# Kernel optimization log

Hardware: AMD Instinct MI355X
Metric: run time of the kernel (lower is better)

Reference implementation:

```python
import jax, jax.numpy as jnp
import numpy as np

QMAX = 127.0  # int8 symmetric
EPS = 1e-8

def _quant_dequant(v, axis):
    # symmetric int8 fake-quant along `axis` (per-row for weights, per-token for acts)
    scale = jnp.max(jnp.abs(v), axis=axis, keepdims=True) / QMAX
    scale = jnp.maximum(scale, EPS)
    q = jnp.clip(jnp.round(v / scale), -QMAX, QMAX)
    return q * scale

def _ste(v, axis):
    # straight-through estimator: identity gradient through quantization
    return v + jax.lax.stop_gradient(_quant_dequant(v, axis) - v)

def setup_inputs() -> dict:
    key = jax.random.key(0)
    k1, k2, k3 = jax.random.split(key, 3)
    H, I = 2048, 5632
    x = jax.random.normal(k1, (4, 2048, H), dtype=jnp.float32)
    # nn.Linear weight layout: [out_features, in_features]
    w_gate_up = jax.random.normal(k2, (2 * I, H), dtype=jnp.float32) * (H ** -0.5)
    w_down = jax.random.normal(k3, (H, I), dtype=jnp.float32) * (I ** -0.5)
    return {"x": x, "w_gate_up": w_gate_up, "w_down": w_down}

def reference(x, w_gate_up, w_down):
    I = w_down.shape[1]
    # QLinear #1: quantize act per-token, weight per-out-channel, dequant matmul
    xq = _ste(x, axis=-1)                       # [B,S,H]
    w1q = _ste(w_gate_up, axis=-1)              # [2I,H]
    gate_up = jnp.einsum('bsh,oh->bso', xq, w1q)  # [B,S,2I]
    gate, up = gate_up[..., :I], gate_up[..., I:]
    h = jax.nn.silu(gate) * up                  # SwiGLU, [B,S,I]
    # QLinear #2
    hq = _ste(h, axis=-1)
    w2q = _ste(w_down, axis=-1)                 # [H,I]
    return jnp.einsum('bsi,oi->bso', hq, w2q)   # [B,S,H]
```

## Files before the change

kernel.cpp:

```cpp
#include <hip/hip_runtime.h>
#include <hip/hip_bf16.h>
#include <stdint.h>

#define H_DIM 2048
#define I_DIM 5632
#define M_DIM 8192
#define N1_DIM (2 * I_DIM)

typedef __attribute__((ext_vector_type(4))) int i32x4;

__device__ __forceinline__ void gload16(const void* g, void* l) {
  __builtin_amdgcn_global_load_lds(
      reinterpret_cast<const __attribute__((address_space(1))) uint32_t*>(
          reinterpret_cast<uintptr_t>(g)),
      reinterpret_cast<__attribute__((address_space(3))) uint32_t*>(
          reinterpret_cast<uintptr_t>(l)),
      16, 0, 0);
}

__global__ __launch_bounds__(256) void quant_rows_f32(
    const float* __restrict__ in, int8_t* __restrict__ q,
    float* __restrict__ scl, int rowlen) {
  const int row = blockIdx.x;
  const int tid = threadIdx.x;
  const float* rp = in + (size_t)row * rowlen;
  float m = 0.f;
  for (int i = tid * 4; i < rowlen; i += 1024) {
    const float4 v = *reinterpret_cast<const float4*>(rp + i);
    m = fmaxf(m, fmaxf(fmaxf(fabsf(v.x), fabsf(v.y)),
                       fmaxf(fabsf(v.z), fabsf(v.w))));
  }
#pragma unroll
  for (int o = 32; o; o >>= 1) m = fmaxf(m, __shfl_xor(m, o));
  __shared__ float wm[4];
  if ((tid & 63) == 0) wm[tid >> 6] = m;
  __syncthreads();
  m = fmaxf(fmaxf(wm[0], wm[1]), fmaxf(wm[2], wm[3]));
  const float scale = fmaxf(m / 127.0f, 1e-8f);
  const float inv = 1.0f / scale;
  if (tid == 0) scl[row] = scale;
  int8_t* qp = q + (size_t)row * rowlen;
  for (int i = tid * 4; i < rowlen; i += 1024) {
    const float4 v = *reinterpret_cast<const float4*>(rp + i);
    const int a = (int)rintf(fminf(fmaxf(v.x * inv, -127.f), 127.f));
    const int b = (int)rintf(fminf(fmaxf(v.y * inv, -127.f), 127.f));
    const int c = (int)rintf(fminf(fmaxf(v.z * inv, -127.f), 127.f));
    const int d = (int)rintf(fminf(fmaxf(v.w * inv, -127.f), 127.f));
    *reinterpret_cast<int*>(qp + i) =
        (a & 255) | ((b & 255) << 8) | ((c & 255) << 16) | (d << 24);
  }
}

__global__ __launch_bounds__(256) void quant_h_rows(
    const __hip_bfloat16* __restrict__ h, const int* __restrict__ amax,
    int8_t* __restrict__ q, float* __restrict__ scl) {
  const int row = blockIdx.x;
  const int tid = threadIdx.x;
  const float scale = fmaxf(__int_as_float(amax[row]) / 127.0f, 1e-8f);
  const float inv = 1.0f / scale;
  if (tid == 0) scl[row] = scale;
  const __hip_bfloat16* rp = h + (size_t)row * I_DIM;
  int8_t* qp = q + (size_t)row * I_DIM;
  for (int i = tid * 8; i < I_DIM; i += 2048) {
    const uint4 v = *reinterpret_cast<const uint4*>(rp + i);
    const uint32_t w[4] = {v.x, v.y, v.z, v.w};
    int pk0 = 0, pk1 = 0;
#pragma unroll
    for (int j = 0; j < 8; ++j) {
      const float f =
          __uint_as_float(((w[j >> 1] >> ((j & 1) * 16)) & 0xffffu) << 16);
      const int qv = (int)rintf(fminf(fmaxf(f * inv, -127.f), 127.f));
      if (j < 4) pk0 |= (qv & 255) << ((j & 3) * 8);
      else       pk1 |= (qv & 255) << ((j & 3) * 8);
    }
    *reinterpret_cast<int2*>(qp + i) = make_int2(pk0, pk1);
  }
}

__global__ __launch_bounds__(256) void gemm1_silu(
    const int8_t* __restrict__ qx, const float* __restrict__ sx,
    const int8_t* __restrict__ qw, const float* __restrict__ sw,
    __hip_bfloat16* __restrict__ h, int* __restrict__ hmax) {
  __shared__ int8_t lds[65536];
  const int tid = threadIdx.x;
  const int lane = tid & 63;
  const int wid = tid >> 6;
  const int bn = blockIdx.x;
  const int bm = blockIdx.y;

  const int lr = lane >> 3;
  const int swz = ((lane & 7) ^ lr) << 4;
  const size_t loff = (size_t)lr * H_DIM + swz;

  const int8_t* Ag  = qx + (size_t)(bm * 128 + wid * 32) * H_DIM;
  const int8_t* Bgg = qw + (size_t)(bn * 64 + wid * 16) * H_DIM;
  const int8_t* Bug = qw + (size_t)(I_DIM + bn * 64 + wid * 16) * H_DIM;

  const int wr = wid >> 1, wc = wid & 1;
  const int c16 = lane & 15;
  const int kq = lane >> 4;
  const int r7 = lane & 7;

  i32x4 accg[4][2] = {};
  i32x4 accu[4][2] = {};

  auto stage = [&](int buf, int kt) {
    const int kb = kt * 128;
#pragma unroll
    for (int i = 0; i < 4; ++i)
      gload16(Ag + (size_t)i * 8 * H_DIM + kb + loff,
              lds + buf * 16384 + (wid * 32 + i * 8) * 128);
#pragma unroll
    for (int i = 0; i < 2; ++i)
      gload16(Bgg + (size_t)i * 8 * H_DIM + kb + loff,
              lds + 32768 + buf * 8192 + (wid * 16 + i * 8) * 128);
#pragma unroll
    for (int i = 0; i < 2; ++i)
      gload16(Bug + (size_t)i * 8 * H_DIM + kb + loff,
              lds + 49152 + buf * 8192 + (wid * 16 + i * 8) * 128);
  };

  stage(0, 0);
  __syncthreads();
  const int KT = H_DIM / 128;
  for (int kt = 0; kt < KT; ++kt) {
    const int cur = kt & 1;
    if (kt + 1 < KT) stage(cur ^ 1, kt + 1);
    const int8_t* Ab  = lds + cur * 16384;
    const int8_t* Bgb = lds + 32768 + cur * 8192;
    const int8_t* Bub = lds + 49152 + cur * 8192;
#pragma unroll
    for (int kk = 0; kk < 2; ++kk) {
      const int slot = ((kk * 4 + kq) ^ r7) << 4;
      i32x4 a[4], bg[2], bu[2];
#pragma unroll
      for (int m = 0; m < 4; ++m)
        a[m] = *reinterpret_cast<const i32x4*>(
            Ab + (wr * 64 + m * 16 + c16) * 128 + slot);
#pragma unroll
      for (int n = 0; n < 2; ++n) {
        bg[n] = *reinterpret_cast<const i32x4*>(
            Bgb + (wc * 32 + n * 16 + c16) * 128 + slot);
        bu[n] = *reinterpret_cast<const i32x4*>(
            Bub + (wc * 32 + n * 16 + c16) * 128 + slot);
      }
#pragma unroll
      for (int m = 0; m < 4; ++m)
#pragma unroll
        for (int n = 0; n < 2; ++n) {
          accg[m][n] =
              __builtin_amdgcn_mfma_i32_16x16x64_i8(a[m], bg[n], accg[m][n], 0, 0, 0);
          accu[m][n] =
              __builtin_amdgcn_mfma_i32_16x16x64_i8(a[m], bu[n], accu[m][n], 0, 0, 0);
        }
    }
    __syncthreads();
  }

  const int row0 = bm * 128 + wr * 64;
  const int col0 = bn * 64 + wc * 32;
#pragma unroll
  for (int m = 0; m < 4; ++m) {
#pragma unroll
    for (int r = 0; r < 4; ++r) {
      const int row = row0 + m * 16 + kq * 4 + r;
      const float sxr = sx[row];
      float rmax = 0.f;
#pragma unroll
      for (int n = 0; n < 2; ++n) {
        const int col = col0 + n * 16 + c16;
        const float g = (float)accg[m][n][r] * (sxr * sw[col]);
        const float u = (float)accu[m][n][r] * (sxr * sw[I_DIM + col]);
        const float hv = g / (1.f + __expf(-g)) * u;
        h[(size_t)row * I_DIM + col] = __float2bfloat16(hv);
        rmax = fmaxf(rmax, fabsf(hv));
      }
#pragma unroll
      for (int o = 1; o < 16; o <<= 1) rmax = fmaxf(rmax, __shfl_xor(rmax, o));
      if (c16 == 0) atomicMax(hmax + row, __float_as_int(rmax));
    }
  }
}

__global__ __launch_bounds__(256) void gemm2(
    const int8_t* __restrict__ qh, const float* __restrict__ sh,
    const int8_t* __restrict__ qw, const float* __restrict__ sw,
    float* __restrict__ out) {
  __shared__ int8_t lds[65536];
  const int tid = threadIdx.x;
  const int lane = tid & 63;
  const int wid = tid >> 6;
  const int bn = blockIdx.x;
  const int bm = blockIdx.y;

  const int lr = lane >> 3;
  const int swz = ((lane & 7) ^ lr) << 4;
  const size_t loff = (size_t)lr * I_DIM + swz;

  const int8_t* Ag = qh + (size_t)(bm * 128 + wid * 32) * I_DIM;
  const int8_t* Bg = qw + (size_t)(bn * 128 + wid * 32) * I_DIM;

  const int wr = wid >> 1, wc = wid & 1;
  const int c16 = lane & 15;
  const int kq = lane >> 4;
  const int r7 = lane & 7;

  i32x4 acc[4][4] = {};

  auto stage = [&](int buf, int kt) {
    const int kb = kt * 128;
#pragma unroll
    for (int i = 0; i < 4; ++i)
      gload16(Ag + (size_t)i * 8 * I_DIM + kb + loff,
              lds + buf * 16384 + (wid * 32 + i * 8) * 128);
#pragma unroll
    for (int i = 0; i < 4; ++i)
      gload16(Bg + (size_t)i * 8 * I_DIM + kb + loff,
              lds + 32768 + buf * 16384 + (wid * 32 + i * 8) * 128);
  };

  stage(0, 0);
  __syncthreads();
  const int KT = I_DIM / 128;
  for (int kt = 0; kt < KT; ++kt) {
    const int cur = kt & 1;
    if (kt + 1 < KT) stage(cur ^ 1, kt + 1);
    const int8_t* Ab = lds + cur * 16384;
    const int8_t* Bb = lds + 32768 + cur * 16384;
#pragma unroll
    for (int kk = 0; kk < 2; ++kk) {
      const int slot = ((kk * 4 + kq) ^ r7) << 4;
      i32x4 a[4], b[4];
#pragma unroll
      for (int m = 0; m < 4; ++m)
        a[m] = *reinterpret_cast<const i32x4*>(
            Ab + (wr * 64 + m * 16 + c16) * 128 + slot);
#pragma unroll
      for (int n = 0; n < 4; ++n)
        b[n] = *reinterpret_cast<const i32x4*>(
            Bb + (wc * 64 + n * 16 + c16) * 128 + slot);
#pragma unroll
      for (int m = 0; m < 4; ++m)
#pragma unroll
        for (int n = 0; n < 4; ++n)
          acc[m][n] =
              __builtin_amdgcn_mfma_i32_16x16x64_i8(a[m], b[n], acc[m][n], 0, 0, 0);
    }
    __syncthreads();
  }

  const int row0 = bm * 128 + wr * 64;
  const int col0 = bn * 128 + wc * 64;
#pragma unroll
  for (int m = 0; m < 4; ++m) {
#pragma unroll
    for (int r = 0; r < 4; ++r) {
      const int row = row0 + m * 16 + kq * 4 + r;
      const float shr = sh[row];
#pragma unroll
      for (int n = 0; n < 4; ++n) {
        const int col = col0 + n * 16 + c16;
        out[(size_t)row * H_DIM + col] = (float)acc[m][n][r] * (shr * sw[col]);
      }
    }
  }
}

extern "C" void kernel_launch(void* const* d_in, const int* in_sizes, int n_in,
                              void* d_out, int out_size, void* d_ws, size_t ws_size,
                              hipStream_t stream) {
  (void)in_sizes; (void)n_in; (void)out_size; (void)ws_size;
  const float* x  = (const float*)d_in[0];
  const float* w1 = (const float*)d_in[1];
  const float* w2 = (const float*)d_in[2];
  float* out = (float*)d_out;

  size_t off = 0;
  auto alloc = [&](size_t n) {
    void* p = (char*)d_ws + off;
    off += (n + 255) & ~(size_t)255;
    return p;
  };
  int8_t* qx  = (int8_t*)alloc((size_t)M_DIM * H_DIM);
  int8_t* qw1 = (int8_t*)alloc((size_t)N1_DIM * H_DIM);
  int8_t* qw2 = (int8_t*)alloc((size_t)H_DIM * I_DIM);
  int8_t* qh  = (int8_t*)alloc((size_t)M_DIM * I_DIM);
  __hip_bfloat16* hb = (__hip_bfloat16*)alloc((size_t)M_DIM * I_DIM * 2);
  float* sx  = (float*)alloc((size_t)M_DIM * 4);
  float* sw1 = (float*)alloc((size_t)N1_DIM * 4);
  float* sw2 = (float*)alloc((size_t)H_DIM * 4);
  float* shs = (float*)alloc((size_t)M_DIM * 4);
  int* hmax  = (int*)alloc((size_t)M_DIM * 4);

  hipMemsetAsync(hmax, 0, (size_t)M_DIM * 4, stream);
  quant_rows_f32<<<M_DIM, 256, 0, stream>>>(x, qx, sx, H_DIM);
  quant_rows_f32<<<N1_DIM, 256, 0, stream>>>(w1, qw1, sw1, H_DIM);
  quant_rows_f32<<<H_DIM, 256, 0, stream>>>(w2, qw2, sw2, I_DIM);
  gemm1_silu<<<dim3(I_DIM / 64, M_DIM / 128), 256, 0, stream>>>(
      qx, sx, qw1, sw1, hb, hmax);
  quant_h_rows<<<M_DIM, 256, 0, stream>>>(hb, hmax, qh, shs);
  gemm2<<<dim3(H_DIM / 128, M_DIM / 128), 256, 0, stream>>>(
      qh, shs, qw2, sw2, out);
}
```

Baseline: 467.7 us.

## Enlarge GEMM tiles to 256x256 with 8 waves and a quarter-split barrier pipeline

Both int8 GEMMs move from 128-row tiles with 4 waves to 256x256 output tiles (gate and up halves together in gemm1) computed by 512-thread blocks. Each K step is split into four MFMA quadrants, with global-to-LDS staging of the next halves interleaved between barriers and priority raised around MFMA bursts. A 1D grid with an XCD-aware block swizzle replaces the 2D grid, aiming to raise operand reuse and L2 locality. The trade-offs are 128KB of LDS per block, a large accumulator register footprint, and many extra barriers.

```diff
diff --git a/kernel.cpp b/kernel.cpp
--- a/kernel.cpp
+++ b/kernel.cpp
@@ -17,6 +17,13 @@
           reinterpret_cast<uintptr_t>(l)),
       16, 0, 0);
 }
+
+#define BAR()                                \
+  do {                                       \
+    asm volatile("" ::: "memory");           \
+    __builtin_amdgcn_s_barrier();            \
+    asm volatile("" ::: "memory");           \
+  } while (0)
 
 __global__ __launch_bounds__(256) void quant_rows_f32(
     const float* __restrict__ in, int8_t* __restrict__ q,
@@ -77,190 +84,283 @@
   }
 }
 
-__global__ __launch_bounds__(256) void gemm1_silu(
+__global__ __launch_bounds__(512, 2) void gemm1_silu(
     const int8_t* __restrict__ qx, const float* __restrict__ sx,
     const int8_t* __restrict__ qw, const float* __restrict__ sw,
     __hip_bfloat16* __restrict__ h, int* __restrict__ hmax) {
-  __shared__ int8_t lds[65536];
+  __shared__ int8_t lds[131072];
   const int tid = threadIdx.x;
   const int lane = tid & 63;
   const int wid = tid >> 6;
-  const int bn = blockIdx.x;
-  const int bm = blockIdx.y;
-
-  const int lr = lane >> 3;
-  const int swz = ((lane & 7) ^ lr) << 4;
-  const size_t loff = (size_t)lr * H_DIM + swz;
-
-  const int8_t* Ag  = qx + (size_t)(bm * 128 + wid * 32) * H_DIM;
-  const int8_t* Bgg = qw + (size_t)(bn * 64 + wid * 16) * H_DIM;
-  const int8_t* Bug = qw + (size_t)(I_DIM + bn * 64 + wid * 16) * H_DIM;
-
-  const int wr = wid >> 1, wc = wid & 1;
+  const int wr = wid >> 2;
+  const int wc = wid & 3;
   const int c16 = lane & 15;
   const int kq = lane >> 4;
   const int r7 = lane & 7;
-
-  i32x4 accg[4][2] = {};
-  i32x4 accu[4][2] = {};
-
-  auto stage = [&](int buf, int kt) {
-    const int kb = kt * 128;
-#pragma unroll
-    for (int i = 0; i < 4; ++i)
-      gload16(Ag + (size_t)i * 8 * H_DIM + kb + loff,
-              lds + buf * 16384 + (wid * 32 + i * 8) * 128);
-#pragma unroll
-    for (int i = 0; i < 2; ++i)
-      gload16(Bgg + (size_t)i * 8 * H_DIM + kb + loff,
-              lds + 32768 + buf * 8192 + (wid * 16 + i * 8) * 128);
-#pragma unroll
-    for (int i = 0; i < 2; ++i)
-      gload16(Bug + (size_t)i * 8 * H_DIM + kb + loff,
-              lds + 49152 + buf * 8192 + (wid * 16 + i * 8) * 128);
-  };
-
-  stage(0, 0);
-  __syncthreads();
+  const int lr = lane >> 3;
+  const int sslot = ((lane & 7) ^ lr) << 4;
+  const int sl0 = (kq ^ r7) << 4;
+  const int sl1 = ((4 + kq) ^ r7) << 4;
+
+  const int nwg = gridDim.x;
+  const int id = blockIdx.x;
+  const int swz = (id & 7) * (nwg >> 3) + (id >> 3);
+  const int NBN = I_DIM / 128;
+  const int bm = swz / NBN;
+  const int bn = swz % NBN;
+
+  const size_t goffA = (size_t)(bm * 256 + wid * 8 + lr) * H_DIM + sslot;
+  const size_t goffG = (size_t)(bn * 128 + wid * 8 + lr) * H_DIM + sslot;
+  const size_t goffU = goffG + (size_t)I_DIM * H_DIM;
+  const int ldsAw = wid * 8 * 128;
+  const int ldsBw = 65536 + wid * 8 * 128;
+
+  i32x4 acc[2][4][2][2] = {};
+
+#define STAGE_A1(half, t)                                                      \
+  do {                                                                         \
+    const int _b = ((t) & 1) * 32768;                                          \
+    _Pragma("unroll") for (int ld = 0; ld < 2; ++ld)                           \
+        gload16(qx + goffA + (size_t)((half)*128 + ld * 64) * H_DIM +          \
+                    (size_t)(t) * 128,                                         \
+                lds + _b + ldsAw + ((half)*128 + ld * 64) * 128);              \
+  } while (0)
+
+#define STAGE_B1(half, t)                                                      \
+  do {                                                                         \
+    const int _b = ((t) & 1) * 32768;                                          \
+    const int8_t* _s = (half) ? (qw + goffU) : (qw + goffG);                   \
+    _Pragma("unroll") for (int ld = 0; ld < 2; ++ld)                           \
+        gload16(_s + (size_t)(ld * 64) * H_DIM + (size_t)(t) * 128,            \
+                lds + _b + ldsBw + ((half)*128 + ld * 64) * 128);              \
+  } while (0)
+
+#define LOAD_A1(MH)                                                            \
+  do {                                                                         \
+    _Pragma("unroll") for (int m = 0; m < 4; ++m) {                            \
+      const int ar = (MH)*128 + wr * 64 + m * 16 + c16;                        \
+      a[m][0] = *reinterpret_cast<const i32x4*>(lds + cb + ar * 128 + sl0);    \
+      a[m][1] = *reinterpret_cast<const i32x4*>(lds + cb + ar * 128 + sl1);    \
+    }                                                                          \
+  } while (0)
+
+#define LOAD_B1(NH)                                                            \
+  do {                                                                         \
+    _Pragma("unroll") for (int n = 0; n < 2; ++n) {                            \
+      const int br = (NH)*128 + wc * 32 + n * 16 + c16;                        \
+      b[NH][n][0] =                                                            \
+          *reinterpret_cast<const i32x4*>(lds + 65536 + cb + br * 128 + sl0);  \
+      b[NH][n][1] =                                                            \
+          *reinterpret_cast<const i32x4*>(lds + 65536 + cb + br * 128 + sl1);  \
+    }                                                                          \
+  } while (0)
+
+#define MFMA_Q1(MH, NH)                                                        \
+  do {                                                                         \
+    __builtin_amdgcn_s_setprio(1);                                             \
+    _Pragma("unroll") for (int kk = 0; kk < 2; ++kk)                           \
+        _Pragma("unroll") for (int m = 0; m < 4; ++m)                          \
+            _Pragma("unroll") for (int n = 0; n < 2; ++n) acc[MH][m][NH][n] =  \
+        __builtin_amdgcn_mfma_i32_16x16x64_i8(a[m][kk], b[NH][n][kk],          \
+                                              acc[MH][m][NH][n], 0, 0, 0);     \
+    __builtin_amdgcn_s_setprio(0);                                             \
+  } while (0)
+
   const int KT = H_DIM / 128;
-  for (int kt = 0; kt < KT; ++kt) {
-    const int cur = kt & 1;
-    if (kt + 1 < KT) stage(cur ^ 1, kt + 1);
-    const int8_t* Ab  = lds + cur * 16384;
-    const int8_t* Bgb = lds + 32768 + cur * 8192;
-    const int8_t* Bub = lds + 49152 + cur * 8192;
-#pragma unroll
-    for (int kk = 0; kk < 2; ++kk) {
-      const int slot = ((kk * 4 + kq) ^ r7) << 4;
-      i32x4 a[4], bg[2], bu[2];
-#pragma unroll
-      for (int m = 0; m < 4; ++m)
-        a[m] = *reinterpret_cast<const i32x4*>(
-            Ab + (wr * 64 + m * 16 + c16) * 128 + slot);
-#pragma unroll
-      for (int n = 0; n < 2; ++n) {
-        bg[n] = *reinterpret_cast<const i32x4*>(
-            Bgb + (wc * 32 + n * 16 + c16) * 128 + slot);
-        bu[n] = *reinterpret_cast<const i32x4*>(
-            Bub + (wc * 32 + n * 16 + c16) * 128 + slot);
+  STAGE_A1(0, 0); STAGE_B1(0, 0); STAGE_A1(1, 0); STAGE_B1(1, 0);
+  STAGE_A1(0, 1); STAGE_B1(0, 1);
+  asm volatile("s_waitcnt vmcnt(4)" ::: "memory");
+  BAR();
+
+#pragma unroll 1
+  for (int t = 0; t < KT; ++t) {
+    const int cb = (t & 1) * 32768;
+    i32x4 a[4][2], b[2][2][2];
+    LOAD_A1(0); LOAD_B1(0);
+    if (t + 1 < KT) STAGE_A1(1, t + 1);
+    BAR();
+    MFMA_Q1(0, 0);
+    BAR();
+    LOAD_B1(1);
+    if (t + 1 < KT) STAGE_B1(1, t + 1);
+    BAR();
+    MFMA_Q1(0, 1);
+    BAR();
+    LOAD_A1(1);
+    if (t + 2 < KT) STAGE_A1(0, t + 2);
+    BAR();
+    MFMA_Q1(1, 0);
+    BAR();
+    if (t + 2 < KT) STAGE_B1(0, t + 2);
+    BAR();
+    MFMA_Q1(1, 1);
+    if (t + 2 < KT) asm volatile("s_waitcnt vmcnt(4)" ::: "memory");
+    else            asm volatile("s_waitcnt vmcnt(0)" ::: "memory");
+    BAR();
+  }
+
+  const int row0 = bm * 256 + wr * 64 + kq * 4;
+  const int col0 = bn * 128 + wc * 32 + c16;
+#pragma unroll
+  for (int mh = 0; mh < 2; ++mh) {
+#pragma unroll
+    for (int m = 0; m < 4; ++m) {
+#pragma unroll
+      for (int r = 0; r < 4; ++r) {
+        const int row = row0 + mh * 128 + m * 16 + r;
+        const float sxr = sx[row];
+        float rmax = 0.f;
+#pragma unroll
+        for (int n = 0; n < 2; ++n) {
+          const int col = col0 + n * 16;
+          const float g = (float)acc[mh][m][0][n][r] * (sxr * sw[col]);
+          const float u = (float)acc[mh][m][1][n][r] * (sxr * sw[I_DIM + col]);
+          const float hv = g / (1.f + __expf(-g)) * u;
+          h[(size_t)row * I_DIM + col] = __float2bfloat16(hv);
+          rmax = fmaxf(rmax, fabsf(hv));
+        }
+#pragma unroll
+        for (int o = 1; o < 16; o <<= 1)
+          rmax = fmaxf(rmax, __shfl_xor(rmax, o));
+        if (c16 == 0) atomicMax(hmax + row, __float_as_int(rmax));
       }
-#pragma unroll
-      for (int m = 0; m < 4; ++m)
-#pragma unroll
-        for (int n = 0; n < 2; ++n) {
-          accg[m][n] =
-              __builtin_amdgcn_mfma_i32_16x16x64_i8(a[m], bg[n], accg[m][n], 0, 0, 0);
-          accu[m][n] =
-              __builtin_amdgcn_mfma_i32_16x16x64_i8(a[m], bu[n], accu[m][n], 0, 0, 0);
-        }
     }
-    __syncthreads();
-  }
-
-  const int row0 = bm * 128 + wr * 64;
-  const int col0 = bn * 64 + wc * 32;
-#pragma unroll
-  for (int m = 0; m < 4; ++m) {
-#pragma unroll
-    for (int r = 0; r < 4; ++r) {
-      const int row = row0 + m * 16 + kq * 4 + r;
-      const float sxr = sx[row];
-      float rmax = 0.f;
-#pragma unroll
-      for (int n = 0; n < 2; ++n) {
-        const int col = col0 + n * 16 + c16;
-        const float g = (float)accg[m][n][r] * (sxr * sw[col]);
-        const float u = (float)accu[m][n][r] * (sxr * sw[I_DIM + col]);
-        const float hv = g / (1.f + __expf(-g)) * u;
-        h[(size_t)row * I_DIM + col] = __float2bfloat16(hv);
-        rmax = fmaxf(rmax, fabsf(hv));
-      }
-#pragma unroll
-      for (int o = 1; o < 16; o <<= 1) rmax = fmaxf(rmax, __shfl_xor(rmax, o));
-      if (c16 == 0) atomicMax(hmax + row, __float_as_int(rmax));
-    }
-  }
-}
-
-__global__ __launch_bounds__(256) void gemm2(
+  }
+}
+
+__global__ __launch_bounds__(512, 2) void gemm2(
     const int8_t* __restrict__ qh, const float* __restrict__ sh,
     const int8_t* __restrict__ qw, const float* __restrict__ sw,
     float* __restrict__ out) {
-  __shared__ int8_t lds[65536];
+  __shared__ int8_t lds[131072];
   const int tid = threadIdx.x;
   const int lane = tid & 63;
   const int wid = tid >> 6;
-  const int bn = blockIdx.x;
-  const int bm = blockIdx.y;
-
-  const int lr = lane >> 3;
-  const int swz = ((lane & 7) ^ lr) << 4;
-  const size_t loff = (size_t)lr * I_DIM + swz;
-
-  const int8_t* Ag = qh + (size_t)(bm * 128 + wid * 32) * I_DIM;
-  const int8_t* Bg = qw + (size_t)(bn * 128 + wid * 32) * I_DIM;
-
-  const int wr = wid >> 1, wc = wid & 1;
+  const int wr = wid >> 2;
+  const int wc = wid & 3;
   const int c16 = lane & 15;
   const int kq = lane >> 4;
   const int r7 = lane & 7;
-
-  i32x4 acc[4][4] = {};
-
-  auto stage = [&](int buf, int kt) {
-    const int kb = kt * 128;
-#pragma unroll
-    for (int i = 0; i < 4; ++i)
-      gload16(Ag + (size_t)i * 8 * I_DIM + kb + loff,
-              lds + buf * 16384 + (wid * 32 + i * 8) * 128);
-#pragma unroll
-    for (int i = 0; i < 4; ++i)
-      gload16(Bg + (size_t)i * 8 * I_DIM + kb + loff,
-              lds + 32768 + buf * 16384 + (wid * 32 + i * 8) * 128);
-  };
-
-  stage(0, 0);
-  __syncthreads();
+  const int lr = lane >> 3;
+  const int sslot = ((lane & 7) ^ lr) << 4;
+  const int sl0 = (kq ^ r7) << 4;
+  const int sl1 = ((4 + kq) ^ r7) << 4;
+
+  const int nwg = gridDim.x;
+  const int id = blockIdx.x;
+  const int swz = (id & 7) * (nwg >> 3) + (id >> 3);
+  const int NBN = H_DIM / 256;
+  const int bm = swz / NBN;
+  const int bn = swz % NBN;
+
+  const size_t goffA = (size_t)(bm * 256 + wid * 8 + lr) * I_DIM + sslot;
+  const size_t goffB = (size_t)(bn * 256 + wid * 8 + lr) * I_DIM + sslot;
+  const int ldsAw = wid * 8 * 128;
+  const int ldsBw = 65536 + wid * 8 * 128;
+
+  i32x4 acc[2][4][2][2] = {};
+
+#define STAGE_A2(half, t)                                                      \
+  do {                                                                         \
+    const int _b = ((t) & 1) * 32768;                                          \
+    _Pragma("unroll") for (int ld = 0; ld < 2; ++ld)                           \
+        gload16(qh + goffA + (size_t)((half)*128 + ld * 64) * I_DIM +          \
+                    (size_t)(t) * 128,                                         \
+                lds + _b + ldsAw + ((half)*128 + ld * 64) * 128);              \
+  } while (0)
+
+#define STAGE_B2(half, t)                                                      \
+  do {                                                                         \
+    const int _b = ((t) & 1) * 32768;                                          \
+    _Pragma("unroll") for (int ld = 0; ld < 2; ++ld)                           \
+        gload16(qw + goffB + (size_t)((half)*128 + ld * 64) * I_DIM +          \
+                    (size_t)(t) * 128,                                         \
+                lds + _b + ldsBw + ((half)*128 + ld * 64) * 128);              \
+  } while (0)
+
+#define LOAD_A2(MH)                                                            \
+  do {                                                                         \
+    _Pragma("unroll") for (int m = 0; m < 4; ++m) {                            \
+      const int ar = (MH)*128 + wr * 64 + m * 16 + c16;                        \
+      a[m][0] = *reinterpret_cast<const i32x4*>(lds + cb + ar * 128 + sl0);    \
+      a[m][1] = *reinterpret_cast<const i32x4*>(lds + cb + ar * 128 + sl1);    \
+    }                                                                          \
+  } while (0)
+
+#define LOAD_B2(NH)                                                            \
+  do {                                                                         \
+    _Pragma("unroll") for (int n = 0; n < 2; ++n) {                            \
+      const int br = (NH)*128 + wc * 32 + n * 16 + c16;                        \
+      b[NH][n][0] =                                                            \
+          *reinterpret_cast<const i32x4*>(lds + 65536 + cb + br * 128 + sl0);  \
+      b[NH][n][1] =                                                            \
+          *reinterpret_cast<const i32x4*>(lds + 65536 + cb + br * 128 + sl1);  \
+    }                                                                          \
+  } while (0)
+
+#define MFMA_Q2(MH, NH)                                                        \
+  do {                                                                         \
+    __builtin_amdgcn_s_setprio(1);                                             \
+    _Pragma("unroll") for (int kk = 0; kk < 2; ++kk)                           \
+        _Pragma("unroll") for (int m = 0; m < 4; ++m)                          \
+            _Pragma("unroll") for (int n = 0; n < 2; ++n) acc[MH][m][NH][n] =  \
+        __builtin_amdgcn_mfma_i32_16x16x64_i8(a[m][kk], b[NH][n][kk],          \
+                                              acc[MH][m][NH][n], 0, 0, 0);     \
+    __builtin_amdgcn_s_setprio(0);                                             \
+  } while (0)
+
   const int KT = I_DIM / 128;
-  for (int kt = 0; kt < KT; ++kt) {
-    const int cur = kt & 1;
-    if (kt + 1 < KT) stage(cur ^ 1, kt + 1);
-    const int8_t* Ab = lds + cur * 16384;
-    const int8_t* Bb = lds + 32768 + cur * 16384;
-#pragma unroll
-    for (int kk = 0; kk < 2; ++kk) {
-      const int slot = ((kk * 4 + kq) ^ r7) << 4;
-      i32x4 a[4], b[4];
-#pragma unroll
-      for (int m = 0; m < 4; ++m)
-        a[m] = *reinterpret_cast<const i32x4*>(
-            Ab + (wr * 64 + m * 16 + c16) * 128 + slot);
-#pragma unroll
-      for (int n = 0; n < 4; ++n)
-        b[n] = *reinterpret_cast<const i32x4*>(
-            Bb + (wc * 64 + n * 16 + c16) * 128 + slot);
-#pragma unroll
-      for (int m = 0; m < 4; ++m)
-#pragma unroll
-        for (int n = 0; n < 4; ++n)
-          acc[m][n] =
-              __builtin_amdgcn_mfma_i32_16x16x64_i8(a[m], b[n], acc[m][n], 0, 0, 0);
-    }
-    __syncthreads();
-  }
-
-  const int row0 = bm * 128 + wr * 64;
-  const int col0 = bn * 128 + wc * 64;
-#pragma unroll
-  for (int m = 0; m < 4; ++m) {
-#pragma unroll
-    for (int r = 0; r < 4; ++r) {
-      const int row = row0 + m * 16 + kq * 4 + r;
-      const float shr = sh[row];
-#pragma unroll
-      for (int n = 0; n < 4; ++n) {
-        const int col = col0 + n * 16 + c16;
-        out[(size_t)row * H_DIM + col] = (float)acc[m][n][r] * (shr * sw[col]);
+  STAGE_A2(0, 0); STAGE_B2(0, 0); STAGE_A2(1, 0); STAGE_B2(1, 0);
+  STAGE_A2(0, 1); STAGE_B2(0, 1);
+  asm volatile("s_waitcnt vmcnt(4)" ::: "memory");
+  BAR();
+
+#pragma unroll 1
+  for (int t = 0; t < KT; ++t) {
+    const int cb = (t & 1) * 32768;
+    i32x4 a[4][2], b[2][2][2];
+    LOAD_A2(0); LOAD_B2(0);
+    if (t + 1 < KT) STAGE_A2(1, t + 1);
+    BAR();
+    MFMA_Q2(0, 0);
+    BAR();
+    LOAD_B2(1);
+    if (t + 1 < KT) STAGE_B2(1, t + 1);
+    BAR();
+    MFMA_Q2(0, 1);
+    BAR();
+    LOAD_A2(1);
+    if (t + 2 < KT) STAGE_A2(0, t + 2);
+    BAR();
+    MFMA_Q2(1, 0);
+    BAR();
+    if (t + 2 < KT) STAGE_B2(0, t + 2);
+    BAR();
+    MFMA_Q2(1, 1);
+    if (t + 2 < KT) asm volatile("s_waitcnt vmcnt(4)" ::: "memory");
+    else            asm volatile("s_waitcnt vmcnt(0)" ::: "memory");
+    BAR();
+  }
+
+  const int row0 = bm * 256 + wr * 64 + kq * 4;
+  const int col0 = bn * 256 + wc * 32 + c16;
+#pragma unroll
+  for (int mh = 0; mh < 2; ++mh) {
+#pragma unroll
+    for (int m = 0; m < 4; ++m) {
+#pragma unroll
+      for (int r = 0; r < 4; ++r) {
+        const int row = row0 + mh * 128 + m * 16 + r;
+        const float shr = sh[row];
+#pragma unroll
+        for (int nh = 0; nh < 2; ++nh) {
+#pragma unroll
+          for (int n = 0; n < 2; ++n) {
+            const int col = col0 + nh * 128 + n * 16;
+            out[(size_t)row * H_DIM + col] =
+                (float)acc[mh][m][nh][n][r] * (shr * sw[col]);
+          }
+        }
       }
     }
   }
@@ -296,9 +396,9 @@
   quant_rows_f32<<<M_DIM, 256, 0, stream>>>(x, qx, sx, H_DIM);
   quant_rows_f32<<<N1_DIM, 256, 0, stream>>>(w1, qw1, sw1, H_DIM);
   quant_rows_f32<<<H_DIM, 256, 0, stream>>>(w2, qw2, sw2, I_DIM);
-  gemm1_silu<<<dim3(I_DIM / 64, M_DIM / 128), 256, 0, stream>>>(
+  gemm1_silu<<<(M_DIM / 256) * (I_DIM / 128), 512, 0, stream>>>(
       qx, sx, qw1, sw1, hb, hmax);
   quant_h_rows<<<M_DIM, 256, 0, stream>>>(hb, hmax, qh, shs);
-  gemm2<<<dim3(H_DIM / 128, M_DIM / 128), 256, 0, stream>>>(
+  gemm2<<<(M_DIM / 256) * (H_DIM / 256), 512, 0, stream>>>(
       qh, shs, qw2, sw2, out);
 }
```

Result: no change. 459.4 us (-1.8%).
